# Optimization experiments

Hardware: AMD Instinct MI355X
Metric: run time of the kernel (lower is better)

The kernel has to match this reference:

```python
import jax, jax.numpy as jnp
import numpy as np

HEADS = 16
D_MODEL = 1024
D_K = D_MODEL // HEADS
SEQ = 2048
BSZ = 2


def softmax_one(x, axis):
    # softmax with an extra +1 in the denominator ("attention off" slot)
    x = x - jnp.max(x, axis=axis, keepdims=True)
    ex = jnp.exp(x)
    return ex / (1.0 + jnp.sum(ex, axis=axis, keepdims=True))


def setup_inputs() -> dict:
    key = jax.random.key(0)
    ks = jax.random.split(key, 7)
    s = 1.0 / np.sqrt(D_MODEL)
    return {
        "x": jax.random.normal(ks[0], (SEQ, BSZ, D_MODEL), dtype=jnp.float32),
        "Wq": jax.random.normal(ks[1], (D_MODEL, D_MODEL), dtype=jnp.float32) * s,
        "bq": jnp.zeros((D_MODEL,), dtype=jnp.float32),
        "Wk": jax.random.normal(ks[2], (D_MODEL, D_MODEL), dtype=jnp.float32) * s,
        "bk": jnp.zeros((D_MODEL,), dtype=jnp.float32),
        "Wv": jax.random.normal(ks[3], (D_MODEL, D_MODEL), dtype=jnp.float32) * s,
        "bv": jnp.zeros((D_MODEL,), dtype=jnp.float32),
    }


def reference(x, Wq, bq, Wk, bk, Wv, bv):
    S, B, D = x.shape
    q = (x @ Wq.T + bq).reshape(S, B, HEADS, D_K)
    k = (x @ Wk.T + bk).reshape(S, B, HEADS, D_K)
    v = (x @ Wv.T + bv).reshape(S, B, HEADS, D_K)
    # [i, j, b, h] full score tensor, scaled by sqrt(d_k)
    scores = jnp.einsum('ibhd,jbhd->ijbh', q, k) / np.sqrt(D_K).astype(np.float32)
    causal = jnp.tril(jnp.ones((S, S), dtype=bool))[:, :, None, None]
    scores = jnp.where(causal, scores, -jnp.inf)
    attn = softmax_one(scores, axis=1)  # softmax over key axis j with +1 denom
    out = jnp.einsum('ijbh,jbhd->ibhd', attn, v)
    return out.reshape(S, B, D)
```

## Files before the change

### kernel.cpp

```cpp
#include <hip/hip_runtime.h>

#define SEQ 2048
#define BSZ 2
#define NH 16
#define DKD 64
#define DM 1024
#define NROW (SEQ*BSZ)
#define KDIM 1024

typedef __attribute__((ext_vector_type(8))) short bf16x8;
typedef __attribute__((ext_vector_type(4))) float floatx4;

__device__ __forceinline__ unsigned short f2b(float f) {
  unsigned int u = __builtin_bit_cast(unsigned int, f);
  u += 0x7fffu + ((u >> 16) & 1u);
  return (unsigned short)(u >> 16);
}

__device__ __forceinline__ void async_copy16(void* lds, const void* g) {
  __builtin_amdgcn_global_load_lds(
      (__attribute__((address_space(1))) void*)(void*)g,
      (__attribute__((address_space(3))) void*)lds, 16, 0, 0);
}

__device__ __forceinline__ floatx4 mfma16(bf16x8 a, bf16x8 b, floatx4 c) {
  return __builtin_amdgcn_mfma_f32_16x16x32_bf16(a, b, c, 0, 0, 0);
}

__global__ __launch_bounds__(256) void cvt_kernel(
    const float* __restrict__ x, const float* __restrict__ Wq,
    const float* __restrict__ Wk, const float* __restrict__ Wv,
    ushort* __restrict__ xbf, ushort* __restrict__ wbf) {
  size_t tid = (size_t)blockIdx.x * 256 + threadIdx.x;
  size_t i4 = tid * 4;
  const float* src;
  const size_t NX = (size_t)NROW * KDIM;
  ushort* dst;
  size_t off;
  if (i4 < NX) {
    src = x; off = i4; dst = xbf + i4;
  } else {
    size_t wix = i4 - NX;
    int proj = (int)(wix >> 20);
    src = proj == 0 ? Wq : (proj == 1 ? Wk : Wv);
    off = wix & 1048575u;
    dst = wbf + wix;
  }
  float4 v = *(const float4*)(src + off);
  ushort4 o;
  o.x = f2b(v.x); o.y = f2b(v.y); o.z = f2b(v.z); o.w = f2b(v.w);
  *(ushort4*)dst = o;
}

__global__ __launch_bounds__(256, 2) void gemm_qkv(
    const ushort* __restrict__ xbf, const ushort* __restrict__ wbf,
    const float* __restrict__ bq, const float* __restrict__ bk,
    const float* __restrict__ bvv,
    ushort* __restrict__ Qs, ushort* __restrict__ Ks, ushort* __restrict__ Vt) {
  __shared__ ushort Al[128 * 32];
  __shared__ ushort Bl[128 * 32];
  const int t = threadIdx.x;
  const int w = t >> 6, l = t & 63;
  const int wr = w >> 1, wc = w & 1;
  const int lane15 = l & 15, quad = l >> 4;
  const int rb = blockIdx.x, cb = blockIdx.y;
  const ushort* Ag = xbf + (size_t)rb * 128 * KDIM;
  const ushort* Bg = wbf + (size_t)cb * 128 * KDIM;
  const int rsub = l >> 2, c2 = (l & 3) * 8;

  floatx4 acc[4][4];
  #pragma unroll
  for (int i = 0; i < 4; ++i)
    #pragma unroll
    for (int j = 0; j < 4; ++j) acc[i][j] = (floatx4){0.f, 0.f, 0.f, 0.f};

  for (int kk = 0; kk < KDIM; kk += 32) {
    __syncthreads();
    #pragma unroll
    for (int half = 0; half < 2; ++half) {
      int rloc = w * 32 + half * 16;
      async_copy16(&Al[rloc * 32], Ag + (size_t)(rloc + rsub) * KDIM + kk + c2);
      async_copy16(&Bl[rloc * 32], Bg + (size_t)(rloc + rsub) * KDIM + kk + c2);
    }
    __syncthreads();
    bf16x8 af[4], bfr[4];
    #pragma unroll
    for (int mt = 0; mt < 4; ++mt)
      af[mt] = *(const bf16x8*)&Al[(wr * 64 + mt * 16 + lane15) * 32 + quad * 8];
    #pragma unroll
    for (int nt = 0; nt < 4; ++nt)
      bfr[nt] = *(const bf16x8*)&Bl[(wc * 64 + nt * 16 + lane15) * 32 + quad * 8];
    #pragma unroll
    for (int mt = 0; mt < 4; ++mt)
      #pragma unroll
      for (int nt = 0; nt < 4; ++nt)
        acc[mt][nt] = mfma16(af[mt], bfr[nt], acc[mt][nt]);
  }

  int proj = (cb * 128) >> 10;
  const float* bias = proj == 0 ? bq : (proj == 1 ? bk : bvv);
  float scale = proj == 0 ? 0.125f * 1.44269504088896f : 1.0f;

  if (proj < 2) {
    ushort* dst = proj == 0 ? Qs : Ks;
    #pragma unroll
    for (int nt = 0; nt < 4; ++nt) {
      int mcol = cb * 128 + wc * 64 + nt * 16 + lane15;
      int cip = mcol & 1023;
      int h = cip >> 6, dk = cip & 63;
      float bias_v = bias[cip];
      #pragma unroll
      for (int mt = 0; mt < 4; ++mt) {
        #pragma unroll
        for (int r = 0; r < 4; ++r) {
          int n = rb * 128 + wr * 64 + mt * 16 + quad * 4 + r;
          int s = n >> 1, b = n & 1;
          float val = (acc[mt][nt][r] + bias_v) * scale;
          dst[((size_t)(b * NH + h) * SEQ + s) * DKD + dk] = f2b(val);
        }
      }
    }
  } else {
    #pragma unroll
    for (int nt = 0; nt < 4; ++nt) {
      int mcol = cb * 128 + wc * 64 + nt * 16 + lane15;
      int cip = mcol & 1023;
      int h = cip >> 6, dk = cip & 63;
      float bias_v = bias[cip];
      #pragma unroll
      for (int mt = 0; mt < 4; ++mt) {
        #pragma unroll
        for (int r = 0; r < 4; ++r) {
          int n = rb * 128 + wr * 64 + mt * 16 + quad * 4 + r;
          int s = n >> 1, b = n & 1;
          float val = acc[mt][nt][r] + bias_v;
          Vt[((size_t)(b * NH + h) * DKD + dk) * SEQ + s] = f2b(val);
        }
      }
    }
  }
}

__global__ __launch_bounds__(256, 4) void attn_kernel(
    const ushort* __restrict__ Qs, const ushort* __restrict__ Ks,
    const ushort* __restrict__ Vt, float* __restrict__ out) {
  __shared__ ushort Kl[64 * 72];
  __shared__ ushort Vl[64 * 72];
  __shared__ ushort Pl[4][16 * 72];
  const int t = threadIdx.x;
  const int w = t >> 6, l = t & 63;
  const int lane15 = l & 15, quad = l >> 4;
  const int qt = (blockIdx.x * 13 + blockIdx.y * 7) & 31;
  const int bh = blockIdx.y;
  const int b = bh >> 4, h = bh & 15;
  const int qbase = qt * 64;
  const int qrow = qbase + w * 16 + lane15;

  const ushort* Qg = Qs + ((size_t)bh * SEQ + qrow) * DKD;
  bf16x8 qf0 = *(const bf16x8*)(Qg + quad * 8);
  bf16x8 qf1 = *(const bf16x8*)(Qg + 32 + quad * 8);
  const ushort* Kg = Ks + (size_t)bh * SEQ * DKD;
  const ushort* Vg = Vt + (size_t)bh * DKD * SEQ;

  const int srow = t >> 3;
  const int scol = (t & 7) * 8;

  floatx4 o[4];
  #pragma unroll
  for (int i = 0; i < 4; ++i) o[i] = (floatx4){0.f, 0.f, 0.f, 0.f};
  floatx4 lacc = (floatx4){0.f, 0.f, 0.f, 0.f};
  float m_r[4] = {-1e30f, -1e30f, -1e30f, -1e30f};

  bf16x8 ones;
  #pragma unroll
  for (int j = 0; j < 8; ++j) ones[j] = (short)0x3F80;

  uint4 kr0 = *(const uint4*)(Kg + (size_t)srow * DKD + scol);
  uint4 kr1 = *(const uint4*)(Kg + (size_t)(srow + 32) * DKD + scol);
  uint4 vr0 = *(const uint4*)(Vg + (size_t)srow * SEQ + scol);
  uint4 vr1 = *(const uint4*)(Vg + (size_t)(srow + 32) * SEQ + scol);

  for (int kt = 0; kt <= qt; ++kt) {
    __syncthreads();
    *(uint4*)&Kl[srow * 72 + scol] = kr0;
    *(uint4*)&Kl[(srow + 32) * 72 + scol] = kr1;
    *(uint4*)&Vl[srow * 72 + scol] = vr0;
    *(uint4*)&Vl[(srow + 32) * 72 + scol] = vr1;
    __syncthreads();

    if (kt < qt) {
      const ushort* Kn = Kg + (size_t)(kt + 1) * 64 * DKD;
      const ushort* Vn = Vg + (kt + 1) * 64;
      kr0 = *(const uint4*)(Kn + (size_t)srow * DKD + scol);
      kr1 = *(const uint4*)(Kn + (size_t)(srow + 32) * DKD + scol);
      vr0 = *(const uint4*)(Vn + (size_t)srow * SEQ + scol);
      vr1 = *(const uint4*)(Vn + (size_t)(srow + 32) * SEQ + scol);
    }

    floatx4 sf[4];
    #pragma unroll
    for (int nt = 0; nt < 4; ++nt) {
      floatx4 a = (floatx4){0.f, 0.f, 0.f, 0.f};
      bf16x8 k0 = *(const bf16x8*)&Kl[(nt * 16 + lane15) * 72 + quad * 8];
      bf16x8 k1 = *(const bf16x8*)&Kl[(nt * 16 + lane15) * 72 + 32 + quad * 8];
      a = mfma16(qf0, k0, a);
      a = mfma16(qf1, k1, a);
      sf[nt] = a;
    }

    if (kt == qt) {
      #pragma unroll
      for (int nt = 0; nt < 4; ++nt) {
        int j = kt * 64 + nt * 16 + lane15;
        #pragma unroll
        for (int r = 0; r < 4; ++r) {
          int i = qbase + w * 16 + quad * 4 + r;
          if (j > i) sf[nt][r] = -1e30f;
        }
      }
    }

    float alpha[4];
    #pragma unroll
    for (int r = 0; r < 4; ++r) {
      float v = fmaxf(fmaxf(sf[0][r], sf[1][r]), fmaxf(sf[2][r], sf[3][r]));
      v = fmaxf(v, __shfl_xor(v, 1, 64));
      v = fmaxf(v, __shfl_xor(v, 2, 64));
      v = fmaxf(v, __shfl_xor(v, 4, 64));
      v = fmaxf(v, __shfl_xor(v, 8, 64));
      float mn = fmaxf(m_r[r], v);
      alpha[r] = __builtin_amdgcn_exp2f(m_r[r] - mn);
      m_r[r] = mn;
    }
    ushort* Pw = &Pl[w][0];
    #pragma unroll
    for (int nt = 0; nt < 4; ++nt)
      #pragma unroll
      for (int r = 0; r < 4; ++r) {
        float p = __builtin_amdgcn_exp2f(sf[nt][r] - m_r[r]);
        Pw[(quad * 4 + r) * 72 + nt * 16 + lane15] =
            (ushort)(__builtin_bit_cast(unsigned int, p) >> 16);
      }
    #pragma unroll
    for (int ntd = 0; ntd < 4; ++ntd)
      #pragma unroll
      for (int r = 0; r < 4; ++r) o[ntd][r] *= alpha[r];
    #pragma unroll
    for (int r = 0; r < 4; ++r) lacc[r] *= alpha[r];

    asm volatile("s_waitcnt lgkmcnt(0)" ::: "memory");
    bf16x8 pa0 = *(const bf16x8*)&Pw[lane15 * 72 + quad * 8];
    bf16x8 pa1 = *(const bf16x8*)&Pw[lane15 * 72 + 32 + quad * 8];

    lacc = mfma16(pa0, ones, lacc);
    lacc = mfma16(pa1, ones, lacc);

    #pragma unroll
    for (int ntd = 0; ntd < 4; ++ntd) {
      bf16x8 v0 = *(const bf16x8*)&Vl[(ntd * 16 + lane15) * 72 + quad * 8];
      bf16x8 v1 = *(const bf16x8*)&Vl[(ntd * 16 + lane15) * 72 + 32 + quad * 8];
      o[ntd] = mfma16(pa0, v0, o[ntd]);
      o[ntd] = mfma16(pa1, v1, o[ntd]);
    }
  }

  float inv[4];
  #pragma unroll
  for (int r = 0; r < 4; ++r) inv[r] = 1.0f / (1.0f + lacc[r]);
  #pragma unroll
  for (int ntd = 0; ntd < 4; ++ntd) {
    int d = h * DKD + ntd * 16 + lane15;
    #pragma unroll
    for (int r = 0; r < 4; ++r) {
      int i = qbase + w * 16 + quad * 4 + r;
      out[((size_t)i * BSZ + b) * DM + d] = o[ntd][r] * inv[r];
    }
  }
}

extern "C" void kernel_launch(void* const* d_in, const int* in_sizes, int n_in,
                              void* d_out, int out_size, void* d_ws, size_t ws_size,
                              hipStream_t stream) {
  (void)in_sizes; (void)n_in; (void)out_size; (void)ws_size;
  const float* x  = (const float*)d_in[0];
  const float* Wq = (const float*)d_in[1];
  const float* bq = (const float*)d_in[2];
  const float* Wk = (const float*)d_in[3];
  const float* bk = (const float*)d_in[4];
  const float* Wv = (const float*)d_in[5];
  const float* bv = (const float*)d_in[6];
  float* out = (float*)d_out;

  ushort* xbf = (ushort*)d_out;
  ushort* wbf = (ushort*)((char*)d_out + 8388608);

  char* ws = (char*)d_ws;
  ushort* Qs = (ushort*)(ws);
  ushort* Ks = (ushort*)(ws + 8388608);
  ushort* Vt = (ushort*)(ws + 16777216);

  cvt_kernel<<<dim3(7168), dim3(256), 0, stream>>>(x, Wq, Wk, Wv, xbf, wbf);
  gemm_qkv<<<dim3(32, 24), dim3(256), 0, stream>>>(xbf, wbf, bq, bk, bv, Qs, Ks, Vt);
  attn_kernel<<<dim3(32, 32), dim3(256), 0, stream>>>(Qs, Ks, Vt, out);
}
```

Measured before the change: 178.7 us.

## Pair causal query tiles per block, double-buffer K/V, stage GEMM epilogue in LDS

The attention kernel now processes two query tiles per block (qa and 31-qa), giving each block 33 key tiles and removing causal load imbalance. It also double-buffers K/V in LDS to drop one barrier per iteration and overlap loads with compute. The QKV GEMM epilogue stages results in shared memory so Q/K/V are written with coalesced 16-byte stores instead of scattered 2-byte stores. The cost is more LDS per block, a lower occupancy hint, and half as many attention blocks.

```diff
diff --git a/kernel.cpp b/kernel.cpp
--- a/kernel.cpp
+++ b/kernel.cpp
@@ -59,6 +59,7 @@
     ushort* __restrict__ Qs, ushort* __restrict__ Ks, ushort* __restrict__ Vt) {
   __shared__ ushort Al[128 * 32];
   __shared__ ushort Bl[128 * 32];
+  __shared__ ushort Cl[128 * 136];
   const int t = threadIdx.x;
   const int w = t >> 6, l = t & 63;
   const int wr = w >> 1, wc = w & 1;
@@ -100,70 +101,74 @@
   int proj = (cb * 128) >> 10;
   const float* bias = proj == 0 ? bq : (proj == 1 ? bk : bvv);
   float scale = proj == 0 ? 0.125f * 1.44269504088896f : 1.0f;
-
-  if (proj < 2) {
+  bool isV = (proj == 2);
+
+  #pragma unroll
+  for (int nt = 0; nt < 4; ++nt) {
+    int c = wc * 64 + nt * 16 + lane15;
+    int cip = (cb * 128 + c) & 1023;
+    float bias_v = bias[cip];
+    #pragma unroll
+    for (int mt = 0; mt < 4; ++mt) {
+      #pragma unroll
+      for (int r = 0; r < 4; ++r) {
+        int n = wr * 64 + mt * 16 + quad * 4 + r;
+        float val = (acc[mt][nt][r] + bias_v) * scale;
+        if (!isV) Cl[n * 136 + c] = f2b(val);
+        else      Cl[c * 136 + (n & 1) * 64 + (n >> 1)] = f2b(val);
+      }
+    }
+  }
+  __syncthreads();
+
+  if (!isV) {
     ushort* dst = proj == 0 ? Qs : Ks;
-    #pragma unroll
-    for (int nt = 0; nt < 4; ++nt) {
-      int mcol = cb * 128 + wc * 64 + nt * 16 + lane15;
-      int cip = mcol & 1023;
-      int h = cip >> 6, dk = cip & 63;
-      float bias_v = bias[cip];
-      #pragma unroll
-      for (int mt = 0; mt < 4; ++mt) {
-        #pragma unroll
-        for (int r = 0; r < 4; ++r) {
-          int n = rb * 128 + wr * 64 + mt * 16 + quad * 4 + r;
-          int s = n >> 1, b = n & 1;
-          float val = (acc[mt][nt][r] + bias_v) * scale;
-          dst[((size_t)(b * NH + h) * SEQ + s) * DKD + dk] = f2b(val);
-        }
-      }
-    }
+    int b = t >> 7;
+    int sl = t & 63;
+    int chunk = (t >> 6) & 1;
+    int n = (sl << 1) | b;
+    int cip = (cb * 128 + chunk * 64) & 1023;
+    int h = cip >> 6;
+    int s = rb * 64 + sl;
+    ushort* g = dst + (((size_t)(b * NH + h) * SEQ + s) * DKD);
+    const uint4* s4 = (const uint4*)&Cl[n * 136 + chunk * 64];
+    #pragma unroll
+    for (int j = 0; j < 8; ++j) *(uint4*)(g + j * 8) = s4[j];
   } else {
-    #pragma unroll
-    for (int nt = 0; nt < 4; ++nt) {
-      int mcol = cb * 128 + wc * 64 + nt * 16 + lane15;
-      int cip = mcol & 1023;
-      int h = cip >> 6, dk = cip & 63;
-      float bias_v = bias[cip];
-      #pragma unroll
-      for (int mt = 0; mt < 4; ++mt) {
-        #pragma unroll
-        for (int r = 0; r < 4; ++r) {
-          int n = rb * 128 + wr * 64 + mt * 16 + quad * 4 + r;
-          int s = n >> 1, b = n & 1;
-          float val = acc[mt][nt][r] + bias_v;
-          Vt[((size_t)(b * NH + h) * DKD + dk) * SEQ + s] = f2b(val);
-        }
-      }
-    }
-  }
-}
-
-__global__ __launch_bounds__(256, 4) void attn_kernel(
+    int c = t >> 1, b = t & 1;
+    int cip = (cb * 128 + c) & 1023;
+    int h = cip >> 6, dk = c & 63;
+    ushort* g = Vt + ((size_t)(b * NH + h) * DKD + dk) * SEQ + rb * 64;
+    const uint4* s4 = (const uint4*)&Cl[c * 136 + b * 64];
+    #pragma unroll
+    for (int j = 0; j < 8; ++j) *(uint4*)(g + j * 8) = s4[j];
+  }
+}
+
+__global__ __launch_bounds__(256, 2) void attn_kernel(
     const ushort* __restrict__ Qs, const ushort* __restrict__ Ks,
     const ushort* __restrict__ Vt, float* __restrict__ out) {
-  __shared__ ushort Kl[64 * 72];
-  __shared__ ushort Vl[64 * 72];
+  __shared__ ushort Kl[2][64 * 72];
+  __shared__ ushort Vl[2][64 * 72];
   __shared__ ushort Pl[4][16 * 72];
   const int t = threadIdx.x;
   const int w = t >> 6, l = t & 63;
   const int lane15 = l & 15, quad = l >> 4;
-  const int qt = (blockIdx.x * 13 + blockIdx.y * 7) & 31;
+  const int qa = blockIdx.x;
   const int bh = blockIdx.y;
   const int b = bh >> 4, h = bh & 15;
-  const int qbase = qt * 64;
-  const int qrow = qbase + w * 16 + lane15;
-
-  const ushort* Qg = Qs + ((size_t)bh * SEQ + qrow) * DKD;
+  const int qtB = 31 - qa;
+
+  const ushort* Kg = Ks + (size_t)bh * SEQ * DKD;
+  const ushort* Vg = Vt + (size_t)bh * DKD * SEQ;
+  const int srow = t >> 3;
+  const int scol = (t & 7) * 8;
+
+  int qt = qa;
+  int qbase = qt * 64;
+  const ushort* Qg = Qs + ((size_t)bh * SEQ + qbase + w * 16 + lane15) * DKD;
   bf16x8 qf0 = *(const bf16x8*)(Qg + quad * 8);
   bf16x8 qf1 = *(const bf16x8*)(Qg + 32 + quad * 8);
-  const ushort* Kg = Ks + (size_t)bh * SEQ * DKD;
-  const ushort* Vg = Vt + (size_t)bh * DKD * SEQ;
-
-  const int srow = t >> 3;
-  const int scol = (t & 7) * 8;
 
   floatx4 o[4];
   #pragma unroll
@@ -175,34 +180,37 @@
   #pragma unroll
   for (int j = 0; j < 8; ++j) ones[j] = (short)0x3F80;
 
-  uint4 kr0 = *(const uint4*)(Kg + (size_t)srow * DKD + scol);
-  uint4 kr1 = *(const uint4*)(Kg + (size_t)(srow + 32) * DKD + scol);
-  uint4 vr0 = *(const uint4*)(Vg + (size_t)srow * SEQ + scol);
-  uint4 vr1 = *(const uint4*)(Vg + (size_t)(srow + 32) * SEQ + scol);
-
-  for (int kt = 0; kt <= qt; ++kt) {
+  #define KT_OF(j) ((j) <= qa ? (j) : (j) - qa - 1)
+
+  uint4 kr0, kr1, vr0, vr1;
+  {
+    int kt0 = 0;
+    kr0 = *(const uint4*)(Kg + (size_t)(kt0 * 64 + srow) * DKD + scol);
+    kr1 = *(const uint4*)(Kg + (size_t)(kt0 * 64 + srow + 32) * DKD + scol);
+    vr0 = *(const uint4*)(Vg + (size_t)srow * SEQ + kt0 * 64 + scol);
+    vr1 = *(const uint4*)(Vg + (size_t)(srow + 32) * SEQ + kt0 * 64 + scol);
+    *(uint4*)&Kl[0][srow * 72 + scol] = kr0;
+    *(uint4*)&Kl[0][(srow + 32) * 72 + scol] = kr1;
+    *(uint4*)&Vl[0][srow * 72 + scol] = vr0;
+    *(uint4*)&Vl[0][(srow + 32) * 72 + scol] = vr1;
+    int kt1 = KT_OF(1);
+    kr0 = *(const uint4*)(Kg + (size_t)(kt1 * 64 + srow) * DKD + scol);
+    kr1 = *(const uint4*)(Kg + (size_t)(kt1 * 64 + srow + 32) * DKD + scol);
+    vr0 = *(const uint4*)(Vg + (size_t)srow * SEQ + kt1 * 64 + scol);
+    vr1 = *(const uint4*)(Vg + (size_t)(srow + 32) * SEQ + kt1 * 64 + scol);
+  }
+
+  for (int it = 0; it <= 32; ++it) {
+    const int cur = it & 1;
+    const int kt = KT_OF(it);
     __syncthreads();
-    *(uint4*)&Kl[srow * 72 + scol] = kr0;
-    *(uint4*)&Kl[(srow + 32) * 72 + scol] = kr1;
-    *(uint4*)&Vl[srow * 72 + scol] = vr0;
-    *(uint4*)&Vl[(srow + 32) * 72 + scol] = vr1;
-    __syncthreads();
-
-    if (kt < qt) {
-      const ushort* Kn = Kg + (size_t)(kt + 1) * 64 * DKD;
-      const ushort* Vn = Vg + (kt + 1) * 64;
-      kr0 = *(const uint4*)(Kn + (size_t)srow * DKD + scol);
-      kr1 = *(const uint4*)(Kn + (size_t)(srow + 32) * DKD + scol);
-      vr0 = *(const uint4*)(Vn + (size_t)srow * SEQ + scol);
-      vr1 = *(const uint4*)(Vn + (size_t)(srow + 32) * SEQ + scol);
-    }
 
     floatx4 sf[4];
     #pragma unroll
     for (int nt = 0; nt < 4; ++nt) {
       floatx4 a = (floatx4){0.f, 0.f, 0.f, 0.f};
-      bf16x8 k0 = *(const bf16x8*)&Kl[(nt * 16 + lane15) * 72 + quad * 8];
-      bf16x8 k1 = *(const bf16x8*)&Kl[(nt * 16 + lane15) * 72 + 32 + quad * 8];
+      bf16x8 k0 = *(const bf16x8*)&Kl[cur][(nt * 16 + lane15) * 72 + quad * 8];
+      bf16x8 k1 = *(const bf16x8*)&Kl[cur][(nt * 16 + lane15) * 72 + 32 + quad * 8];
       a = mfma16(qf0, k0, a);
       a = mfma16(qf1, k1, a);
       sf[nt] = a;
@@ -257,25 +265,55 @@
 
     #pragma unroll
     for (int ntd = 0; ntd < 4; ++ntd) {
-      bf16x8 v0 = *(const bf16x8*)&Vl[(ntd * 16 + lane15) * 72 + quad * 8];
-      bf16x8 v1 = *(const bf16x8*)&Vl[(ntd * 16 + lane15) * 72 + 32 + quad * 8];
+      bf16x8 v0 = *(const bf16x8*)&Vl[cur][(ntd * 16 + lane15) * 72 + quad * 8];
+      bf16x8 v1 = *(const bf16x8*)&Vl[cur][(ntd * 16 + lane15) * 72 + 32 + quad * 8];
       o[ntd] = mfma16(pa0, v0, o[ntd]);
       o[ntd] = mfma16(pa1, v1, o[ntd]);
     }
-  }
-
-  float inv[4];
-  #pragma unroll
-  for (int r = 0; r < 4; ++r) inv[r] = 1.0f / (1.0f + lacc[r]);
-  #pragma unroll
-  for (int ntd = 0; ntd < 4; ++ntd) {
-    int d = h * DKD + ntd * 16 + lane15;
-    #pragma unroll
-    for (int r = 0; r < 4; ++r) {
-      int i = qbase + w * 16 + quad * 4 + r;
-      out[((size_t)i * BSZ + b) * DM + d] = o[ntd][r] * inv[r];
-    }
-  }
+
+    if (it == qa || it == 32) {
+      float inv[4];
+      #pragma unroll
+      for (int r = 0; r < 4; ++r) inv[r] = 1.0f / (1.0f + lacc[r]);
+      #pragma unroll
+      for (int ntd = 0; ntd < 4; ++ntd) {
+        int d = h * DKD + ntd * 16 + lane15;
+        #pragma unroll
+        for (int r = 0; r < 4; ++r) {
+          int i = qbase + w * 16 + quad * 4 + r;
+          out[((size_t)i * BSZ + b) * DM + d] = o[ntd][r] * inv[r];
+        }
+      }
+      if (it == qa) {
+        #pragma unroll
+        for (int i = 0; i < 4; ++i) o[i] = (floatx4){0.f, 0.f, 0.f, 0.f};
+        lacc = (floatx4){0.f, 0.f, 0.f, 0.f};
+        #pragma unroll
+        for (int r = 0; r < 4; ++r) m_r[r] = -1e30f;
+        qt = qtB;
+        qbase = qt * 64;
+        const ushort* Qg2 = Qs + ((size_t)bh * SEQ + qbase + w * 16 + lane15) * DKD;
+        qf0 = *(const bf16x8*)(Qg2 + quad * 8);
+        qf1 = *(const bf16x8*)(Qg2 + 32 + quad * 8);
+      }
+    }
+
+    if (it < 32) {
+      int nxt = cur ^ 1;
+      *(uint4*)&Kl[nxt][srow * 72 + scol] = kr0;
+      *(uint4*)&Kl[nxt][(srow + 32) * 72 + scol] = kr1;
+      *(uint4*)&Vl[nxt][srow * 72 + scol] = vr0;
+      *(uint4*)&Vl[nxt][(srow + 32) * 72 + scol] = vr1;
+      if (it + 2 <= 32) {
+        int kt2 = KT_OF(it + 2);
+        kr0 = *(const uint4*)(Kg + (size_t)(kt2 * 64 + srow) * DKD + scol);
+        kr1 = *(const uint4*)(Kg + (size_t)(kt2 * 64 + srow + 32) * DKD + scol);
+        vr0 = *(const uint4*)(Vg + (size_t)srow * SEQ + kt2 * 64 + scol);
+        vr1 = *(const uint4*)(Vg + (size_t)(srow + 32) * SEQ + kt2 * 64 + scol);
+      }
+    }
+  }
+  #undef KT_OF
 }
 
 extern "C" void kernel_launch(void* const* d_in, const int* in_sizes, int n_in,
@@ -301,5 +339,5 @@
 
   cvt_kernel<<<dim3(7168), dim3(256), 0, stream>>>(x, Wq, Wk, Wv, xbf, wbf);
   gemm_qkv<<<dim3(32, 24), dim3(256), 0, stream>>>(xbf, wbf, bq, bk, bv, Qs, Ks, Vt);
-  attn_kernel<<<dim3(32, 32), dim3(256), 0, stream>>>(Qs, Ks, Vt, out);
-}
+  attn_kernel<<<dim3(16, 32), dim3(256), 0, stream>>>(Qs, Ks, Vt, out);
+}
```

Result: faster. 174.8 us (-2.2%).
